# Kernel tuning notes

Hardware: AMD Instinct MI355X
Metric: run time of the kernel (lower is better)

## Reference

```python
import jax, jax.numpy as jnp
import numpy as np

N_NODES = 100000
N_EDGES = 1600000
IN_FEATS = 128
HIDDEN = 128
NUM_CLASSES = 4


def setup_inputs() -> dict:
    key = jax.random.key(0)
    ks = jax.random.split(key, 8)
    features = jax.random.normal(ks[0], (N_NODES, IN_FEATS), dtype=jnp.float32)
    src = jax.random.randint(ks[1], (N_EDGES,), 0, N_NODES, dtype=jnp.int64)
    dst = jax.random.randint(ks[2], (N_EDGES,), 0, N_NODES, dtype=jnp.int64)
    s = 1.0 / np.sqrt(IN_FEATS)
    W1 = jax.random.normal(ks[3], (IN_FEATS, HIDDEN), dtype=jnp.float32) * s
    b1 = jnp.zeros((HIDDEN,), dtype=jnp.float32)
    W2 = jax.random.normal(ks[4], (HIDDEN, HIDDEN), dtype=jnp.float32) * s
    b2 = jnp.zeros((HIDDEN,), dtype=jnp.float32)
    Wc = jax.random.normal(ks[5], (HIDDEN, NUM_CLASSES), dtype=jnp.float32) * s
    bc = jnp.zeros((NUM_CLASSES,), dtype=jnp.float32)
    return {"features": features, "src": src, "dst": dst,
            "W1": W1, "b1": b1, "W2": W2, "b2": b2, "Wc": Wc, "bc": bc}


def _graph_conv(x, W, b, src, dst, n_nodes, activation=True):
    # DGL GraphConv, norm='both': D_out^{-1/2} A^T D_in... i.e. symmetric norm.
    ones = jnp.ones((src.shape[0],), dtype=x.dtype)
    deg_out = jnp.clip(jax.ops.segment_sum(ones, src, num_segments=n_nodes), 1.0)
    deg_in = jnp.clip(jax.ops.segment_sum(ones, dst, num_segments=n_nodes), 1.0)
    # scale sources, project (in >= out so matmul first, math-equivalent), gather-scatter
    h = (x * (deg_out ** -0.5)[:, None]) @ W            # [N, out]
    msg = h[src]                                         # [E, out] gather
    agg = jax.ops.segment_sum(msg, dst, num_segments=n_nodes)  # [N, out] scatter-add
    h = agg * (deg_in ** -0.5)[:, None] + b
    return jax.nn.relu(h) if activation else h


def reference(features, src, dst, W1, b1, W2, b2, Wc, bc):
    # eval-mode forward: dropout is identity
    n = features.shape[0]
    h = _graph_conv(features, W1, b1, src, dst, n, activation=True)
    h = _graph_conv(h, W2, b2, src, dst, n, activation=True)
    return h @ Wc + bc  # [N, num_classes] logits
```

## Files before the change

### kernel.cpp

```cpp
#include <hip/hip_runtime.h>
#include <hip/hip_fp16.h>
#include <math.h>

#define N_NODES 100000
#define N_EDGES 1600000
#define F 128
#define NBUK 196
#define BSH 9
#define BSZ 512
#define CAP 10240

typedef _Float16 half8 __attribute__((ext_vector_type(8)));
typedef float    f32x4 __attribute__((ext_vector_type(4)));

__global__ __launch_bounds__(256) void init_pack(int* __restrict__ curD,
                                                 int* __restrict__ degS,
                                                 _Float16* __restrict__ padrow,
                                                 const float* __restrict__ W1,
                                                 const float* __restrict__ W2,
                                                 _Float16* __restrict__ hi1,
                                                 _Float16* __restrict__ lo1,
                                                 _Float16* __restrict__ hi2,
                                                 _Float16* __restrict__ lo2)
{
    int t = threadIdx.x;
    if (blockIdx.x == 0) {
        if (t < NBUK) curD[t] = t * CAP;
        if (t < 16) reinterpret_cast<int4*>(padrow)[t] = make_int4(0, 0, 0, 0);
        return;
    }
    if (blockIdx.x >= 129) {
        int i = (blockIdx.x - 129) * 256 + t;
        if (i < 25000) reinterpret_cast<int4*>(degS)[i] = make_int4(0, 0, 0, 0);
        return;
    }
    int gidx = (blockIdx.x - 1) * 256 + t;
    const float* W = (gidx < 16384) ? W1 : W2;
    _Float16* hi = (gidx < 16384) ? hi1 : hi2;
    _Float16* lo = (gidx < 16384) ? lo1 : lo2;
    int idx = gidx & 16383;
    int f = idx >> 9, r = idx & 511;
    int l = r >> 3, j = r & 7;
    int kc = f >> 3, ct = f & 7;
    int k = kc * 32 + (l >> 4) * 8 + j;
    int n = ct * 16 + (l & 15);
    float w = W[k * 128 + n];
    _Float16 h = (_Float16)w;
    hi[idx] = h;
    lo[idx] = (_Float16)(w - (float)h);
}

__global__ __launch_bounds__(512) void part_gemm1(const int* __restrict__ src,
                                                  const int* __restrict__ dst,
                                                  int* __restrict__ curD,
                                                  int* __restrict__ degS,
                                                  int* __restrict__ bukD,
                                                  const float* __restrict__ X,
                                                  const _Float16* __restrict__ Whi,
                                                  const _Float16* __restrict__ Wlo,
                                                  _Float16* __restrict__ Y, int N)
{
    __shared__ int hd[NBUK], bd[NBUK], cd[NBUK];
    const int tid = threadIdx.x;

    if (blockIdx.x < NBUK) {
        const int chunk = (((N_EDGES + NBUK - 1) / NBUK) + 3) & ~3;
        const int beg = blockIdx.x * chunk;
        const int end = min(beg + chunk, N_EDGES);
        if (beg >= end) return;
        if (tid < NBUK) { hd[tid] = 0; cd[tid] = 0; }
        __syncthreads();
        const int b4 = beg >> 2, e4 = end >> 2;
        for (int i = b4 + tid; i < e4; i += 512) {
            int4 d = reinterpret_cast<const int4*>(dst)[i];
            int4 s = reinterpret_cast<const int4*>(src)[i];
            atomicAdd(&hd[d.x >> BSH], 1); atomicAdd(&hd[d.y >> BSH], 1);
            atomicAdd(&hd[d.z >> BSH], 1); atomicAdd(&hd[d.w >> BSH], 1);
            atomicAdd(&degS[s.x], 1); atomicAdd(&degS[s.y], 1);
            atomicAdd(&degS[s.z], 1); atomicAdd(&degS[s.w], 1);
        }
        __syncthreads();
        if (tid < NBUK)
            bd[tid] = hd[tid] ? atomicAdd(&curD[tid], hd[tid]) : 0;
        __syncthreads();
        for (int e = beg + tid; e < end; e += 512) {
            int d = dst[e], s = src[e];
            int bin = d >> BSH;
            int r = atomicAdd(&cd[bin], 1);
            bukD[bd[bin] + r] = ((d & 511) << 17) | s;
        }
        return;
    }

    const int l = tid & 63, w = tid >> 6;
    const int quad = l >> 4, m = l & 15;
    const int row0 = (blockIdx.x - NBUK) * 256;
    const half8* Bh = reinterpret_cast<const half8*>(Whi);
    const half8* Bl = reinterpret_cast<const half8*>(Wlo);

    f32x4 acc[2][8] = {};

    for (int kc = 0; kc < 4; kc++) {
        half8 ah[2];
        #pragma unroll
        for (int rt = 0; rt < 2; rt++) {
            int grow = row0 + w * 32 + rt * 16 + m;
            float4 xa = make_float4(0.f, 0.f, 0.f, 0.f), xb = xa;
            if (grow < N) {
                const float4* Xp = reinterpret_cast<const float4*>(X) + (size_t)grow * 32 + kc * 8 + quad * 2;
                xa = Xp[0]; xb = Xp[1];
            }
            ah[rt][0] = (_Float16)xa.x; ah[rt][1] = (_Float16)xa.y;
            ah[rt][2] = (_Float16)xa.z; ah[rt][3] = (_Float16)xa.w;
            ah[rt][4] = (_Float16)xb.x; ah[rt][5] = (_Float16)xb.y;
            ah[rt][6] = (_Float16)xb.z; ah[rt][7] = (_Float16)xb.w;
        }
        #pragma unroll
        for (int ct = 0; ct < 8; ct++) {
            int f = kc * 8 + ct;
            half8 bh = Bh[f * 64 + l];
            half8 bl = Bl[f * 64 + l];
            #pragma unroll
            for (int rt = 0; rt < 2; rt++) {
                acc[rt][ct] = __builtin_amdgcn_mfma_f32_16x16x32_f16(ah[rt], bh, acc[rt][ct], 0, 0, 0);
                acc[rt][ct] = __builtin_amdgcn_mfma_f32_16x16x32_f16(ah[rt], bl, acc[rt][ct], 0, 0, 0);
            }
        }
    }

    #pragma unroll
    for (int rt = 0; rt < 2; rt++) {
        #pragma unroll
        for (int r = 0; r < 4; r++) {
            int grow = row0 + w * 32 + rt * 16 + quad * 4 + r;
            if (grow < N) {
                #pragma unroll
                for (int ct = 0; ct < 8; ct++)
                    Y[(size_t)grow * 128 + ct * 16 + m] = (_Float16)(acc[rt][ct][r]);
            }
        }
    }
}

__global__ __launch_bounds__(512) void csr_wv(const int* __restrict__ bukD,
                                              const int* __restrict__ curD,
                                              const int* __restrict__ degS,
                                              int* __restrict__ row_ptr,
                                              float* __restrict__ sin_,
                                              int* __restrict__ col,
                                              float* __restrict__ wv)
{
    __shared__ int h[BSZ], sc[BSZ], cur[BSZ];
    const int tid = threadIdx.x;
    const int n0 = blockIdx.x << BSH;
    const int lo = blockIdx.x * CAP, hi = curD[blockIdx.x];
    h[tid] = 0;
    __syncthreads();
    for (int i = lo + tid; i < hi; i += 512)
        atomicAdd(&h[((unsigned)bukD[i]) >> 17], 1);
    __syncthreads();
    int own = h[tid];
    int own4 = (own + 3) & ~3;
    sc[tid] = own4;
    __syncthreads();
    for (int off = 1; off < 512; off <<= 1) {
        int u = (tid >= off) ? sc[tid - off] : 0;
        __syncthreads();
        sc[tid] += u;
        __syncthreads();
    }
    int ex = sc[tid] - own4;
    cur[tid] = ex;
    int node = n0 + tid;
    if (node < N_NODES) {
        row_ptr[2 * node]     = lo + ex;
        row_ptr[2 * node + 1] = lo + ex + own4;
        sin_[node] = rsqrtf((float)max(own, 1));
    }
    __syncthreads();
    for (int i = lo + tid; i < hi; i += 512) {
        int p = bukD[i];
        int s = p & 0x1FFFF;
        int r = atomicAdd(&cur[((unsigned)p) >> 17], 1);
        col[lo + r] = s;
        wv[lo + r]  = rsqrtf((float)max(degS[s], 1));
    }
    for (int k = own; k < own4; k++) {
        col[lo + ex + k] = N_NODES;
        wv[lo + ex + k]  = 0.f;
    }
}

#define ACCW(vv, ww) \
    a0 = fmaf(ww, (float)vv[0], a0); a1 = fmaf(ww, (float)vv[1], a1); \
    a2 = fmaf(ww, (float)vv[2], a2); a3 = fmaf(ww, (float)vv[3], a3); \
    a4 = fmaf(ww, (float)vv[4], a4); a5 = fmaf(ww, (float)vv[5], a5); \
    a6 = fmaf(ww, (float)vv[6], a6); a7 = fmaf(ww, (float)vv[7], a7);

#define ACCU(vv) \
    a0 += (float)vv[0]; a1 += (float)vv[1]; a2 += (float)vv[2]; a3 += (float)vv[3]; \
    a4 += (float)vv[4]; a5 += (float)vv[5]; a6 += (float)vv[6]; a7 += (float)vv[7];

__global__ __launch_bounds__(256) void gather_agg_s(const _Float16* __restrict__ Hh,
                                                    const int* __restrict__ row_ptr,
                                                    const int* __restrict__ col,
                                                    const float* __restrict__ wv,
                                                    const float* __restrict__ sin_,
                                                    const float* __restrict__ bias,
                                                    _Float16* __restrict__ Yh, int N)
{
    const int sub  = threadIdx.x & 15;
    const int node = blockIdx.x * 16 + (threadIdx.x >> 4);
    if (node >= N) return;
    const int beg = row_ptr[2 * node], end = row_ptr[2 * node + 1];
    const half8* __restrict__ H8 = reinterpret_cast<const half8*>(Hh);

    float a0 = 0.f, a1 = 0.f, a2 = 0.f, a3 = 0.f, a4 = 0.f, a5 = 0.f, a6 = 0.f, a7 = 0.f;
    int i = beg;
    for (; i + 8 <= end; i += 8) {
        int4 ca = *reinterpret_cast<const int4*>(col + i);
        int4 cb = *reinterpret_cast<const int4*>(col + i + 4);
        float4 wa = *reinterpret_cast<const float4*>(wv + i);
        float4 wb = *reinterpret_cast<const float4*>(wv + i + 4);
        half8 v0 = H8[((size_t)ca.x << 4) | sub];
        half8 v1 = H8[((size_t)ca.y << 4) | sub];
        half8 v2 = H8[((size_t)ca.z << 4) | sub];
        half8 v3 = H8[((size_t)ca.w << 4) | sub];
        half8 v4 = H8[((size_t)cb.x << 4) | sub];
        half8 v5 = H8[((size_t)cb.y << 4) | sub];
        half8 v6 = H8[((size_t)cb.z << 4) | sub];
        half8 v7 = H8[((size_t)cb.w << 4) | sub];
        ACCW(v0, wa.x) ACCW(v1, wa.y) ACCW(v2, wa.z) ACCW(v3, wa.w)
        ACCW(v4, wb.x) ACCW(v5, wb.y) ACCW(v6, wb.z) ACCW(v7, wb.w)
    }
    if (i < end) {
        int4 ca = *reinterpret_cast<const int4*>(col + i);
        float4 wa = *reinterpret_cast<const float4*>(wv + i);
        half8 v0 = H8[((size_t)ca.x << 4) | sub];
        half8 v1 = H8[((size_t)ca.y << 4) | sub];
        half8 v2 = H8[((size_t)ca.z << 4) | sub];
        half8 v3 = H8[((size_t)ca.w << 4) | sub];
        ACCW(v0, wa.x) ACCW(v1, wa.y) ACCW(v2, wa.z) ACCW(v3, wa.w)
    }
    float scn = sin_[node];
    const float4* B4 = reinterpret_cast<const float4*>(bias);
    float4 bA = B4[2 * sub], bB = B4[2 * sub + 1];
    half8 o;
    o[0] = (_Float16)fmaxf(fmaf(a0, scn, bA.x), 0.f);
    o[1] = (_Float16)fmaxf(fmaf(a1, scn, bA.y), 0.f);
    o[2] = (_Float16)fmaxf(fmaf(a2, scn, bA.z), 0.f);
    o[3] = (_Float16)fmaxf(fmaf(a3, scn, bA.w), 0.f);
    o[4] = (_Float16)fmaxf(fmaf(a4, scn, bB.x), 0.f);
    o[5] = (_Float16)fmaxf(fmaf(a5, scn, bB.y), 0.f);
    o[6] = (_Float16)fmaxf(fmaf(a6, scn, bB.z), 0.f);
    o[7] = (_Float16)fmaxf(fmaf(a7, scn, bB.w), 0.f);
    reinterpret_cast<half8*>(Yh)[(size_t)node * 16 + sub] = o;
}

__global__ __launch_bounds__(256) void gather_cls(const _Float16* __restrict__ Hh,
                                                  const int* __restrict__ row_ptr,
                                                  const int* __restrict__ col,
                                                  const float* __restrict__ sin_,
                                                  const float* __restrict__ bias,
                                                  const float* __restrict__ Wc,
                                                  const float* __restrict__ bc,
                                                  float* __restrict__ out, int N)
{
    __shared__ float4 Wcs[128];
    for (int t = threadIdx.x; t < 128; t += 256)
        Wcs[t] = reinterpret_cast<const float4*>(Wc)[t];
    __syncthreads();

    const int sub  = threadIdx.x & 15;
    const int node = blockIdx.x * 16 + (threadIdx.x >> 4);
    if (node >= N) return;
    const int beg = row_ptr[2 * node], end = row_ptr[2 * node + 1];
    const half8* __restrict__ H8 = reinterpret_cast<const half8*>(Hh);

    float a0 = 0.f, a1 = 0.f, a2 = 0.f, a3 = 0.f, a4 = 0.f, a5 = 0.f, a6 = 0.f, a7 = 0.f;
    int i = beg;
    for (; i + 8 <= end; i += 8) {
        int4 ca = *reinterpret_cast<const int4*>(col + i);
        int4 cb = *reinterpret_cast<const int4*>(col + i + 4);
        half8 v0 = H8[((size_t)ca.x << 4) | sub];
        half8 v1 = H8[((size_t)ca.y << 4) | sub];
        half8 v2 = H8[((size_t)ca.z << 4) | sub];
        half8 v3 = H8[((size_t)ca.w << 4) | sub];
        half8 v4 = H8[((size_t)cb.x << 4) | sub];
        half8 v5 = H8[((size_t)cb.y << 4) | sub];
        half8 v6 = H8[((size_t)cb.z << 4) | sub];
        half8 v7 = H8[((size_t)cb.w << 4) | sub];
        ACCU(v0) ACCU(v1) ACCU(v2) ACCU(v3)
        ACCU(v4) ACCU(v5) ACCU(v6) ACCU(v7)
    }
    if (i < end) {
        int4 ca = *reinterpret_cast<const int4*>(col + i);
        half8 v0 = H8[((size_t)ca.x << 4) | sub];
        half8 v1 = H8[((size_t)ca.y << 4) | sub];
        half8 v2 = H8[((size_t)ca.z << 4) | sub];
        half8 v3 = H8[((size_t)ca.w << 4) | sub];
        ACCU(v0) ACCU(v1) ACCU(v2) ACCU(v3)
    }
    float scn = sin_[node];
    const float4* B4 = reinterpret_cast<const float4*>(bias);
    float4 bA = B4[2 * sub], bB = B4[2 * sub + 1];
    float h0 = fmaxf(fmaf(a0, scn, bA.x), 0.f);
    float h1 = fmaxf(fmaf(a1, scn, bA.y), 0.f);
    float h2 = fmaxf(fmaf(a2, scn, bA.z), 0.f);
    float h3 = fmaxf(fmaf(a3, scn, bA.w), 0.f);
    float h4 = fmaxf(fmaf(a4, scn, bB.x), 0.f);
    float h5 = fmaxf(fmaf(a5, scn, bB.y), 0.f);
    float h6 = fmaxf(fmaf(a6, scn, bB.z), 0.f);
    float h7 = fmaxf(fmaf(a7, scn, bB.w), 0.f);

    float lx = 0.f, ly = 0.f, lz = 0.f, lw = 0.f;
    float4 w;
    w = Wcs[sub * 8 + 0]; lx = fmaf(h0, w.x, lx); ly = fmaf(h0, w.y, ly); lz = fmaf(h0, w.z, lz); lw = fmaf(h0, w.w, lw);
    w = Wcs[sub * 8 + 1]; lx = fmaf(h1, w.x, lx); ly = fmaf(h1, w.y, ly); lz = fmaf(h1, w.z, lz); lw = fmaf(h1, w.w, lw);
    w = Wcs[sub * 8 + 2]; lx = fmaf(h2, w.x, lx); ly = fmaf(h2, w.y, ly); lz = fmaf(h2, w.z, lz); lw = fmaf(h2, w.w, lw);
    w = Wcs[sub * 8 + 3]; lx = fmaf(h3, w.x, lx); ly = fmaf(h3, w.y, ly); lz = fmaf(h3, w.z, lz); lw = fmaf(h3, w.w, lw);
    w = Wcs[sub * 8 + 4]; lx = fmaf(h4, w.x, lx); ly = fmaf(h4, w.y, ly); lz = fmaf(h4, w.z, lz); lw = fmaf(h4, w.w, lw);
    w = Wcs[sub * 8 + 5]; lx = fmaf(h5, w.x, lx); ly = fmaf(h5, w.y, ly); lz = fmaf(h5, w.z, lz); lw = fmaf(h5, w.w, lw);
    w = Wcs[sub * 8 + 6]; lx = fmaf(h6, w.x, lx); ly = fmaf(h6, w.y, ly); lz = fmaf(h6, w.z, lz); lw = fmaf(h6, w.w, lw);
    w = Wcs[sub * 8 + 7]; lx = fmaf(h7, w.x, lx); ly = fmaf(h7, w.y, ly); lz = fmaf(h7, w.z, lz); lw = fmaf(h7, w.w, lw);

    #pragma unroll
    for (int m = 1; m < 16; m <<= 1) {
        lx += __shfl_xor(lx, m);
        ly += __shfl_xor(ly, m);
        lz += __shfl_xor(lz, m);
        lw += __shfl_xor(lw, m);
    }
    if (sub == 0) {
        float4 bcv = reinterpret_cast<const float4*>(bc)[0];
        float4 r;
        r.x = lx + bcv.x; r.y = ly + bcv.y; r.z = lz + bcv.z; r.w = lw + bcv.w;
        reinterpret_cast<float4*>(out)[node] = r;
    }
}

__global__ __launch_bounds__(256) void gemm_mfma_f16(const _Float16* __restrict__ Xh,
                                                     const _Float16* __restrict__ Whi,
                                                     const _Float16* __restrict__ Wlo,
                                                     const int* __restrict__ degS,
                                                     _Float16* __restrict__ Y, int N)
{
    const int tid = threadIdx.x;
    const int l = tid & 63, w = tid >> 6;
    const int quad = l >> 4, m = l & 15;
    const int row0 = blockIdx.x * 128;
    const half8* Bh = reinterpret_cast<const half8*>(Whi);
    const half8* Bl = reinterpret_cast<const half8*>(Wlo);

    f32x4 acc[2][8] = {};

    for (int kc = 0; kc < 4; kc++) {
        half8 a[2];
        #pragma unroll
        for (int rt = 0; rt < 2; rt++) {
            int grow = row0 + w * 32 + rt * 16 + m;
            half8 z = {};
            a[rt] = (grow < N)
                ? *reinterpret_cast<const half8*>(Xh + (size_t)grow * 128 + kc * 32 + quad * 8)
                : z;
        }
        #pragma unroll
        for (int ct = 0; ct < 8; ct++) {
            int f = kc * 8 + ct;
            half8 bh = Bh[f * 64 + l];
            half8 bl = Bl[f * 64 + l];
            #pragma unroll
            for (int rt = 0; rt < 2; rt++) {
                acc[rt][ct] = __builtin_amdgcn_mfma_f32_16x16x32_f16(a[rt], bh, acc[rt][ct], 0, 0, 0);
                acc[rt][ct] = __builtin_amdgcn_mfma_f32_16x16x32_f16(a[rt], bl, acc[rt][ct], 0, 0, 0);
            }
        }
    }

    #pragma unroll
    for (int rt = 0; rt < 2; rt++) {
        #pragma unroll
        for (int r = 0; r < 4; r++) {
            int grow = row0 + w * 32 + rt * 16 + quad * 4 + r;
            if (grow < N) {
                float s = rsqrtf((float)max(degS[grow], 1));
                #pragma unroll
                for (int ct = 0; ct < 8; ct++)
                    Y[(size_t)grow * 128 + ct * 16 + m] = (_Float16)(acc[rt][ct][r] * s);
            }
        }
    }
}

extern "C" void kernel_launch(void* const* d_in, const int* in_sizes, int n_in,
                              void* d_out, int out_size, void* d_ws, size_t ws_size,
                              hipStream_t stream)
{
    const float* features = (const float*)d_in[0];
    const int*   src      = (const int*)d_in[1];
    const int*   dst      = (const int*)d_in[2];
    const float* W1       = (const float*)d_in[3];
    const float* b1       = (const float*)d_in[4];
    const float* W2       = (const float*)d_in[5];
    const float* b2       = (const float*)d_in[6];
    const float* Wc       = (const float*)d_in[7];
    const float* bc       = (const float*)d_in[8];
    float* out = (float*)d_out;

    char* ws = (char*)d_ws;
    const size_t MB = 1 << 20;
    int* curD  = (int*)(ws + 0);
    _Float16* Whi1 = (_Float16*)(ws + 64 * 1024);
    _Float16* Wlo1 = (_Float16*)(ws + 96 * 1024);
    _Float16* Whi2 = (_Float16*)(ws + 128 * 1024);
    _Float16* Wlo2 = (_Float16*)(ws + 160 * 1024);
    int*   degS    = (int*)(ws + 512 * 1024);
    float* sin_    = (float*)(ws + 1 * MB);
    int*   row_ptr = (int*)(ws + 2 * MB);
    int*   col     = (int*)(ws + 3 * MB);
    float* wv      = (float*)(ws + 11 * MB);
    int*   bukD    = (int*)(ws + 19 * MB);
    _Float16* hMsg = (_Float16*)(ws + 27 * MB);
    _Float16* hA   = (_Float16*)(ws + 52 * MB);

    const int N = N_NODES;
    const int NGB = (N + 15) / 16;

    init_pack<<<227, 256, 0, stream>>>(curD, degS, hMsg + (size_t)N * F,
                                       W1, W2, Whi1, Wlo1, Whi2, Wlo2);

    part_gemm1<<<NBUK + 391, 512, 0, stream>>>(src, dst, curD, degS, bukD,
                                               features, Whi1, Wlo1, hMsg, N);

    csr_wv<<<NBUK, 512, 0, stream>>>(bukD, curD, degS, row_ptr, sin_, col, wv);

    gather_agg_s<<<NGB, 256, 0, stream>>>(hMsg, row_ptr, col, wv, sin_, b1, hA, N);

    gemm_mfma_f16<<<(N + 127) / 128, 256, 0, stream>>>(hA, Whi2, Wlo2, degS, hMsg, N);
    gather_cls<<<NGB, 256, 0, stream>>>(hMsg, row_ptr, col, sin_, b2, Wc, bc, out, N);
}
```

Before: 351.1 us.

## Replace global source-degree atomics with bucketed partition and per-bucket histogram

Instead of global atomicAdd on degS for every edge source, sources are binned into 512-node buckets via shared-memory counters during partitioning, and a new deg_out kernel histograms each bucket in shared memory to produce rsqrt out-degree scales. Downstream kernels read the precomputed float scale instead of recomputing rsqrt from integer degrees. This removes random-address global atomics. In exchange it adds an extra kernel launch and extra bucket writes, and the workspace layout is reshuffled with buffers aliased.

```diff
diff --git a/kernel.cpp b/kernel.cpp
--- a/kernel.cpp
+++ b/kernel.cpp
@@ -14,7 +14,7 @@
 typedef float    f32x4 __attribute__((ext_vector_type(4)));
 
 __global__ __launch_bounds__(256) void init_pack(int* __restrict__ curD,
-                                                 int* __restrict__ degS,
+                                                 int* __restrict__ curS,
                                                  _Float16* __restrict__ padrow,
                                                  const float* __restrict__ W1,
                                                  const float* __restrict__ W2,
@@ -25,13 +25,8 @@
 {
     int t = threadIdx.x;
     if (blockIdx.x == 0) {
-        if (t < NBUK) curD[t] = t * CAP;
+        if (t < NBUK) { curD[t] = t * CAP; curS[t] = t * CAP; }
         if (t < 16) reinterpret_cast<int4*>(padrow)[t] = make_int4(0, 0, 0, 0);
-        return;
-    }
-    if (blockIdx.x >= 129) {
-        int i = (blockIdx.x - 129) * 256 + t;
-        if (i < 25000) reinterpret_cast<int4*>(degS)[i] = make_int4(0, 0, 0, 0);
         return;
     }
     int gidx = (blockIdx.x - 1) * 256 + t;
@@ -53,14 +48,15 @@
 __global__ __launch_bounds__(512) void part_gemm1(const int* __restrict__ src,
                                                   const int* __restrict__ dst,
                                                   int* __restrict__ curD,
-                                                  int* __restrict__ degS,
+                                                  int* __restrict__ curS,
                                                   int* __restrict__ bukD,
+                                                  unsigned short* __restrict__ bukS,
                                                   const float* __restrict__ X,
                                                   const _Float16* __restrict__ Whi,
                                                   const _Float16* __restrict__ Wlo,
                                                   _Float16* __restrict__ Y, int N)
 {
-    __shared__ int hd[NBUK], bd[NBUK], cd[NBUK];
+    __shared__ int hd[NBUK], hs[NBUK], bd[NBUK], bs[NBUK], cd[NBUK], cs[NBUK];
     const int tid = threadIdx.x;
 
     if (blockIdx.x < NBUK) {
@@ -68,7 +64,7 @@
         const int beg = blockIdx.x * chunk;
         const int end = min(beg + chunk, N_EDGES);
         if (beg >= end) return;
-        if (tid < NBUK) { hd[tid] = 0; cd[tid] = 0; }
+        if (tid < NBUK) { hd[tid] = 0; hs[tid] = 0; cd[tid] = 0; cs[tid] = 0; }
         __syncthreads();
         const int b4 = beg >> 2, e4 = end >> 2;
         for (int i = b4 + tid; i < e4; i += 512) {
@@ -76,18 +72,29 @@
             int4 s = reinterpret_cast<const int4*>(src)[i];
             atomicAdd(&hd[d.x >> BSH], 1); atomicAdd(&hd[d.y >> BSH], 1);
             atomicAdd(&hd[d.z >> BSH], 1); atomicAdd(&hd[d.w >> BSH], 1);
-            atomicAdd(&degS[s.x], 1); atomicAdd(&degS[s.y], 1);
-            atomicAdd(&degS[s.z], 1); atomicAdd(&degS[s.w], 1);
+            atomicAdd(&hs[s.x >> BSH], 1); atomicAdd(&hs[s.y >> BSH], 1);
+            atomicAdd(&hs[s.z >> BSH], 1); atomicAdd(&hs[s.w >> BSH], 1);
         }
         __syncthreads();
-        if (tid < NBUK)
+        if (tid < NBUK) {
             bd[tid] = hd[tid] ? atomicAdd(&curD[tid], hd[tid]) : 0;
+            bs[tid] = hs[tid] ? atomicAdd(&curS[tid], hs[tid]) : 0;
+        }
         __syncthreads();
-        for (int e = beg + tid; e < end; e += 512) {
-            int d = dst[e], s = src[e];
-            int bin = d >> BSH;
-            int r = atomicAdd(&cd[bin], 1);
-            bukD[bd[bin] + r] = ((d & 511) << 17) | s;
+        for (int i = b4 + tid; i < e4; i += 512) {
+            int4 d4 = reinterpret_cast<const int4*>(dst)[i];
+            int4 s4 = reinterpret_cast<const int4*>(src)[i];
+            int dd[4] = { d4.x, d4.y, d4.z, d4.w };
+            int ss[4] = { s4.x, s4.y, s4.z, s4.w };
+            #pragma unroll
+            for (int j = 0; j < 4; j++) {
+                int bin = dd[j] >> BSH;
+                int r = atomicAdd(&cd[bin], 1);
+                bukD[bd[bin] + r] = ((dd[j] & 511) << 17) | ss[j];
+                int bin2 = ss[j] >> BSH;
+                int r2 = atomicAdd(&cs[bin2], 1);
+                bukS[bs[bin2] + r2] = (unsigned short)(ss[j] & 511);
+            }
         }
         return;
     }
@@ -142,9 +149,26 @@
     }
 }
 
+__global__ __launch_bounds__(512) void deg_out(const unsigned short* __restrict__ bukS,
+                                               const int* __restrict__ curS,
+                                               float* __restrict__ sout)
+{
+    __shared__ int h[BSZ];
+    const int tid = threadIdx.x;
+    const int n0 = blockIdx.x << BSH;
+    const int lo = blockIdx.x * CAP, hi = curS[blockIdx.x];
+    h[tid] = 0;
+    __syncthreads();
+    for (int i = lo + tid; i < hi; i += 512)
+        atomicAdd(&h[bukS[i]], 1);
+    __syncthreads();
+    int node = n0 + tid;
+    if (node < N_NODES) sout[node] = rsqrtf((float)max(h[tid], 1));
+}
+
 __global__ __launch_bounds__(512) void csr_wv(const int* __restrict__ bukD,
                                               const int* __restrict__ curD,
-                                              const int* __restrict__ degS,
+                                              const float* __restrict__ sout,
                                               int* __restrict__ row_ptr,
                                               float* __restrict__ sin_,
                                               int* __restrict__ col,
@@ -183,7 +207,7 @@
         int s = p & 0x1FFFF;
         int r = atomicAdd(&cur[((unsigned)p) >> 17], 1);
         col[lo + r] = s;
-        wv[lo + r]  = rsqrtf((float)max(degS[s], 1));
+        wv[lo + r]  = sout[s];
     }
     for (int k = own; k < own4; k++) {
         col[lo + ex + k] = N_NODES;
@@ -342,7 +366,7 @@
 __global__ __launch_bounds__(256) void gemm_mfma_f16(const _Float16* __restrict__ Xh,
                                                      const _Float16* __restrict__ Whi,
                                                      const _Float16* __restrict__ Wlo,
-                                                     const int* __restrict__ degS,
+                                                     const float* __restrict__ srow,
                                                      _Float16* __restrict__ Y, int N)
 {
     const int tid = threadIdx.x;
@@ -383,7 +407,7 @@
         for (int r = 0; r < 4; r++) {
             int grow = row0 + w * 32 + rt * 16 + quad * 4 + r;
             if (grow < N) {
-                float s = rsqrtf((float)max(degS[grow], 1));
+                float s = srow[grow];
                 #pragma unroll
                 for (int ct = 0; ct < 8; ct++)
                     Y[(size_t)grow * 128 + ct * 16 + m] = (_Float16)(acc[rt][ct][r] * s);
@@ -410,32 +434,36 @@
     char* ws = (char*)d_ws;
     const size_t MB = 1 << 20;
     int* curD  = (int*)(ws + 0);
+    int* curS  = (int*)(ws + 1024);
     _Float16* Whi1 = (_Float16*)(ws + 64 * 1024);
     _Float16* Wlo1 = (_Float16*)(ws + 96 * 1024);
     _Float16* Whi2 = (_Float16*)(ws + 128 * 1024);
     _Float16* Wlo2 = (_Float16*)(ws + 160 * 1024);
-    int*   degS    = (int*)(ws + 512 * 1024);
+    float* sout    = (float*)(ws + 512 * 1024);
     float* sin_    = (float*)(ws + 1 * MB);
     int*   row_ptr = (int*)(ws + 2 * MB);
     int*   col     = (int*)(ws + 3 * MB);
     float* wv      = (float*)(ws + 11 * MB);
-    int*   bukD    = (int*)(ws + 19 * MB);
-    _Float16* hMsg = (_Float16*)(ws + 27 * MB);
+    _Float16* hMsg = (_Float16*)(ws + 25 * MB);
+    int*   bukD    = (int*)(ws + 52 * MB);
+    unsigned short* bukS = (unsigned short*)(ws + 60 * MB);
     _Float16* hA   = (_Float16*)(ws + 52 * MB);
 
     const int N = N_NODES;
     const int NGB = (N + 15) / 16;
 
-    init_pack<<<227, 256, 0, stream>>>(curD, degS, hMsg + (size_t)N * F,
+    init_pack<<<129, 256, 0, stream>>>(curD, curS, hMsg + (size_t)N * F,
                                        W1, W2, Whi1, Wlo1, Whi2, Wlo2);
 
-    part_gemm1<<<NBUK + 391, 512, 0, stream>>>(src, dst, curD, degS, bukD,
+    part_gemm1<<<NBUK + 391, 512, 0, stream>>>(src, dst, curD, curS, bukD, bukS,
                                                features, Whi1, Wlo1, hMsg, N);
 
-    csr_wv<<<NBUK, 512, 0, stream>>>(bukD, curD, degS, row_ptr, sin_, col, wv);
+    deg_out<<<NBUK, 512, 0, stream>>>(bukS, curS, sout);
+
+    csr_wv<<<NBUK, 512, 0, stream>>>(bukD, curD, sout, row_ptr, sin_, col, wv);
 
     gather_agg_s<<<NGB, 256, 0, stream>>>(hMsg, row_ptr, col, wv, sin_, b1, hA, N);
 
-    gemm_mfma_f16<<<(N + 127) / 128, 256, 0, stream>>>(hA, Whi2, Wlo2, degS, hMsg, N);
+    gemm_mfma_f16<<<(N + 127) / 128, 256, 0, stream>>>(hA, Whi2, Wlo2, sout, hMsg, N);
     gather_cls<<<NGB, 256, 0, stream>>>(hMsg, row_ptr, col, sin_, b2, Wc, bc, out, N);
 }
```

After: 311.9 us. 11.2% less time.
